# Kernel tuning notes

Hardware: AMD Instinct MI355X
Metric: run time of the kernel (lower is better)

The kernel has to match this reference:

```python
import jax, jax.numpy as jnp
import numpy as np

DIM, HEADS, DIM_HEAD = 256, 8, 32  # dim == heads * dim_head
EPS = 1e-5


def setup_inputs() -> dict:
    key = jax.random.key(0)
    ks = jax.random.split(key, 6)
    B, C, H, W = 16, DIM, 64, 64
    x = jax.random.normal(ks[0], (B, C, H, W), dtype=jnp.float32)
    # 1x1 conv weights stored as [out_ch, in_ch]
    w_qkv = jax.random.normal(ks[1], (3 * DIM, DIM), dtype=jnp.float32) * (1.0 / np.sqrt(DIM))
    w_out = jax.random.normal(ks[2], (DIM, DIM), dtype=jnp.float32) * (1.0 / np.sqrt(DIM))
    b_out = jax.random.normal(ks[3], (DIM,), dtype=jnp.float32) * 0.01
    ln_gamma = jnp.ones((DIM,), dtype=jnp.float32)
    ln_beta = jnp.zeros((DIM,), dtype=jnp.float32)
    return {"x": x, "w_qkv": w_qkv, "w_out": w_out, "b_out": b_out,
            "ln_gamma": ln_gamma, "ln_beta": ln_beta}


def _linear_attention(x, w_qkv, w_out, b_out, ln_gamma, ln_beta):
    B, C, H, W = x.shape
    d = C // HEADS
    # 1x1 conv == channel matmul
    qkv = jnp.einsum('bchw,oc->bohw', x, w_qkv)  # [B, 3C, H, W]
    q, k, v = jnp.split(qkv, 3, axis=1)
    # 'b (h d) x y -> b h x y d'
    def split_heads(t):
        t = t.reshape(B, HEADS, d, H, W)
        return t.transpose(0, 1, 3, 4, 2)  # b h x y d
    q, k, v = split_heads(q), split_heads(k), split_heads(v)
    q = jax.nn.softmax(q, axis=-1)   # over d (channel) dim
    k = jax.nn.softmax(k, axis=-2)   # over y spatial axis (faithful to torch dim=-2)
    context = jnp.einsum('bhxyd,bhxye->bhde', k, v)          # [B,H,d,d]
    out = jnp.einsum('bhde,bhxye->bhxyd', context, q)        # [B,H,X,Y,d]
    # 'b h x y d -> b (h d) x y'
    out = out.transpose(0, 1, 4, 2, 3).reshape(B, C, H, W)
    # output 1x1 conv + bias
    out = jnp.einsum('bchw,oc->bohw', out, w_out) + b_out[None, :, None, None]
    # LayerNorm over channel dim (permute to NHWC, norm last axis, permute back)
    y = out.transpose(0, 2, 3, 1)  # b h w c
    mu = jnp.mean(y, axis=-1, keepdims=True)
    var = jnp.var(y, axis=-1, keepdims=True)
    y = (y - mu) / jnp.sqrt(var + EPS) * ln_gamma + ln_beta
    return y.transpose(0, 3, 1, 2)


def reference(x, w_qkv, w_out, b_out, ln_gamma, ln_beta):
    return _linear_attention(x, w_qkv, w_out, b_out, ln_gamma, ln_beta)
```

## Files before the change

kernel.cpp:

```cpp
#include <hip/hip_runtime.h>
#include <hip/hip_bf16.h>

#define NB 16
#define CDIM 256
#define NHEADS 8
#define DH 32
#define NSP 4096
#define O3 768

typedef __bf16 bf16;
typedef bf16 bf16x4 __attribute__((ext_vector_type(4)));
typedef bf16 bf16x8 __attribute__((ext_vector_type(8)));
typedef float f32x4 __attribute__((ext_vector_type(4)));
typedef float f32x16 __attribute__((ext_vector_type(16)));

static __device__ __forceinline__ float bf2f(bf16 x){ return (float)x; }
static __device__ __forceinline__ bf16 f2bf(float x){ return (bf16)x; }

static __device__ __forceinline__ void gld16(const bf16* g, bf16* l){
    __builtin_amdgcn_global_load_lds((const __attribute__((address_space(1))) void*)g,
                                     (__attribute__((address_space(3))) void*)l, 16, 0, 0);
}

__global__ void k_transpose(const float* __restrict__ x, bf16* __restrict__ xT){
    __shared__ bf16 tile[64][72];
    int b = blockIdx.z;
    int c0 = blockIdx.y * 64;
    int n0 = blockIdx.x * 64;
    int t = threadIdx.x;
    const float* xb = x + (size_t)b * CDIM * NSP;
    #pragma unroll
    for (int i = 0; i < 4; ++i){
        int lin = i*256 + t;
        int c = lin >> 4;
        int n4 = (lin & 15) * 4;
        f32x4 f = *(const f32x4*)(xb + (size_t)(c0 + c)*NSP + n0 + n4);
        bf16x4 v4;
        #pragma unroll
        for (int j = 0; j < 4; ++j) v4[j] = f2bf(f[j]);
        *(bf16x4*)&tile[c][n4] = v4;
    }
    __syncthreads();
    bf16* xTb = xT + (size_t)b * NSP * CDIM;
    #pragma unroll
    for (int i = 0; i < 2; ++i){
        int lin = i*256 + t;
        int n = lin >> 3;
        int c8 = (lin & 7) * 8;
        bf16x8 v;
        #pragma unroll
        for (int j = 0; j < 8; ++j) v[j] = tile[c8+j][n];
        *(bf16x8*)(xTb + (size_t)(n0+n)*CDIM + c0 + c8) = v;
    }
}

__global__ void k_wcvt(const float* __restrict__ w, bf16* __restrict__ w2){
    int idx = (blockIdx.x*256 + threadIdx.x) * 4;
    f32x4 f = *(const f32x4*)(w + idx);
    bf16x4 v;
    #pragma unroll
    for (int j=0;j<4;j++) v[j] = f2bf(f[j]);
    *(bf16x4*)(w2 + idx) = v;
}

__global__ __launch_bounds__(1024,4) void k_kvctx(const bf16* __restrict__ w2,
                                                  const bf16* __restrict__ xT,
                                                  float* __restrict__ ctx_p){
    __shared__ union {
        bf16 Bs[32768];
        bf16 cb[32768];
    } sm;
    int bid = blockIdx.x;
    int xcd = bid & 7, slot = bid >> 3;
    int g = xcd*64 + slot;
    int b = g >> 5;
    int ntile = g & 31;
    int n0 = ntile * 128;
    int t = threadIdx.x;
    int wv = t >> 6, lane = t & 63;

    #pragma unroll
    for (int j=0;j<4;j++){
        int base_r = wv*8 + j*2;
        int r = base_r + (lane>>5);
        int c = (lane & 31) ^ (r & 7);
        gld16(xT + ((size_t)b*NSP + n0 + r)*CDIM + c*8, &sm.Bs[(size_t)base_r*256]);
    }
    __syncthreads();

    int brow[8], brx[8];
    #pragma unroll
    for (int ni=0;ni<8;ni++){
        int r = ni*16 + (lane&15);
        brow[ni] = r*32; brx[ni] = r & 7;
    }
    int arow = 256 + wv*32 + (lane&15);
    int acol = (lane>>4)*8;

    f32x4 acc[2][8];
    #pragma unroll
    for (int i=0;i<16;i++) ((f32x4*)acc)[i] = (f32x4){0.f,0.f,0.f,0.f};

    bf16x8 af0 = *(const bf16x8*)(w2 + (size_t)(arow     )*CDIM + acol);
    bf16x8 af1 = *(const bf16x8*)(w2 + (size_t)(arow + 16)*CDIM + acol);
    #pragma unroll
    for (int k0=0;k0<8;k0++){
        bf16x8 an0, an1;
        if (k0 < 7){
            an0 = *(const bf16x8*)(w2 + (size_t)(arow     )*CDIM + (k0+1)*32 + acol);
            an1 = *(const bf16x8*)(w2 + (size_t)(arow + 16)*CDIM + (k0+1)*32 + acol);
        }
        int cbase = (lane>>4) + k0*4;
        bf16x8 bfr[8];
        #pragma unroll
        for (int ni=0;ni<8;ni++)
            bfr[ni] = *(const bf16x8*)&sm.Bs[(size_t)(brow[ni] + (cbase ^ brx[ni]))*8];
        #pragma unroll
        for (int ni=0;ni<8;ni++)
            acc[0][ni] = __builtin_amdgcn_mfma_f32_16x16x32_bf16(af0, bfr[ni], acc[0][ni], 0, 0, 0);
        #pragma unroll
        for (int ni=0;ni<8;ni++)
            acc[1][ni] = __builtin_amdgcn_mfma_f32_16x16x32_bf16(af1, bfr[ni], acc[1][ni], 0, 0, 0);
        af0 = an0; af1 = an1;
    }

    if (wv < 8){
        #pragma unroll
        for (int mi=0;mi<2;mi++)
            #pragma unroll
            for (int r=0;r<4;r++)
                #pragma unroll
                for (int grp=0;grp<2;grp++){
                    float mx = -1e30f;
                    #pragma unroll
                    for (int q=0;q<4;q++) mx = fmaxf(mx, acc[mi][grp*4+q][r]);
                    #pragma unroll
                    for (int msk=1; msk<16; msk<<=1) mx = fmaxf(mx, __shfl_xor(mx, msk, 64));
                    float s = 0.f;
                    #pragma unroll
                    for (int q=0;q<4;q++){
                        float e = __expf(acc[mi][grp*4+q][r] - mx);
                        acc[mi][grp*4+q][r] = e; s += e;
                    }
                    #pragma unroll
                    for (int msk=1; msk<16; msk<<=1) s += __shfl_xor(s, msk, 64);
                    float inv = 1.f/s;
                    #pragma unroll
                    for (int q=0;q<4;q++) acc[mi][grp*4+q][r] *= inv;
                }
    }

    #pragma unroll
    for (int ph=0; ph<2; ++ph){
        __syncthreads();
        if (((wv>>2)&1) == ph){
            int isv  = wv >> 3;
            int w03  = wv & 3;
            int base = isv * 16384;
            #pragma unroll
            for (int mi=0;mi<2;mi++)
                #pragma unroll
                for (int ni=0;ni<8;ni++)
                    #pragma unroll
                    for (int r=0;r<4;r++){
                        int row = w03*32 + mi*16 + (lane>>4)*4 + r;
                        int n = ni*16 + (lane&15);
                        sm.cb[base + row*128 + (((n>>3) ^ (row&15))<<3) + (n&7)] = f2bf(acc[mi][ni][r]);
                    }
        }
        __syncthreads();
        if (wv < 4){
            f32x16 cacc;
            #pragma unroll
            for (int i=0;i<16;i++) cacc[i] = 0.f;
            int rr = wv*32 + (lane&31);
            #pragma unroll
            for (int s=0;s<8;s++){
                int nseg = s*2 + (lane>>5);
                int off = rr*128 + (((nseg ^ (rr&15))<<3));
                bf16x8 ka = *(const bf16x8*)&sm.cb[off];
                bf16x8 vb = *(const bf16x8*)&sm.cb[16384 + off];
                cacc = __builtin_amdgcn_mfma_f32_32x32x16_bf16(ka, vb, cacc, 0, 0, 0);
            }
            float* dst = ctx_p + ((size_t)(b*8 + ph*4 + wv)*32 + ntile)*1024;
            #pragma unroll
            for (int r=0;r<16;r++){
                int d = (r&3) + 8*(r>>2) + 4*(lane>>5);
                dst[d*32 + (lane&31)] = cacc[r];
            }
        }
    }
}

__global__ void k_merge(const float* __restrict__ w_out, const float* __restrict__ ctx_p,
                        bf16* __restrict__ W2){
    __shared__ float ctxs[32][32];
    int bh = blockIdx.x;
    int b = bh >> 3, h = bh & 7;
    int t = threadIdx.x;
    const float* base = ctx_p + (size_t)bh*32*1024;
    #pragma unroll
    for (int i=0;i<4;i++){
        int idx = i*256 + t;
        float s0 = 0.f, s1 = 0.f;
        #pragma unroll
        for (int p=0;p<16;p++){ s0 += base[(2*p)*1024 + idx]; s1 += base[(2*p+1)*1024 + idx]; }
        ((float*)ctxs)[idx] = s0 + s1;
    }
    __syncthreads();
    int o = t;
    const float* wrow = w_out + (size_t)o*CDIM + h*DH;
    float wv[32];
    #pragma unroll
    for (int d=0;d<32;d++) wv[d] = wrow[d];
    bf16* dst = W2 + ((size_t)b*CDIM + o)*CDIM + h*DH;
    #pragma unroll
    for (int g=0;g<4;g++){
        bf16x8 o8;
        #pragma unroll
        for (int jj=0;jj<8;jj++){
            int e = g*8 + jj;
            float s = 0.f;
            #pragma unroll
            for (int d=0;d<32;d++) s += wv[d]*ctxs[d][e];
            o8[jj] = f2bf(s);
        }
        *(bf16x8*)(dst + g*8) = o8;
    }
}

__global__ __launch_bounds__(256,4) void k_qout_ln(const bf16* __restrict__ w2,
                                                   const bf16* __restrict__ xT,
                                                   const bf16* __restrict__ W2,
                                                   const float* __restrict__ bout,
                                                   const float* __restrict__ gamma,
                                                   const float* __restrict__ beta,
                                                   float* __restrict__ out){
    __shared__ union {
        bf16 Bs[8192];
        float Yh[128*33];
    } sm;
    __shared__ float red[2][4][2][16];
    __shared__ float mu_s[32], rstd_s[32];
    int bid = blockIdx.x;
    int xcd = bid & 7, slot = bid >> 3;
    int b  = slot >> 4;
    int n0 = (xcd*16 + (slot & 15)) * 32;
    int t = threadIdx.x, wv = t>>6, lane = t&63;

    const bf16* xTb = xT + (size_t)b * NSP * CDIM;
    #pragma unroll
    for (int j=0;j<4;j++){
        int base_r = wv*8 + j*2;
        int r = base_r + (lane>>5);
        int c = (lane & 31) ^ (r & 7);
        gld16(xTb + (size_t)(n0 + r)*CDIM + c*8, &sm.Bs[(size_t)base_r*256]);
    }
    __syncthreads();

    int brow[2], brx[2];
    #pragma unroll
    for (int ni=0;ni<2;ni++){
        int r = ni*16 + (lane&15);
        brow[ni] = r*32; brx[ni] = r & 7;
    }
    int arow = wv*64 + (lane&15);
    int acol = (lane>>4)*8;

    f32x4 acc[4][2];
    #pragma unroll
    for (int i=0;i<8;i++) ((f32x4*)acc)[i] = (f32x4){0.f,0.f,0.f,0.f};
    {
        bf16x8 af[4], an[4];
        #pragma unroll
        for (int mi=0;mi<4;mi++)
            af[mi] = *(const bf16x8*)(w2 + (size_t)(arow + mi*16)*CDIM + acol);
        #pragma unroll
        for (int k0=0;k0<8;k0++){
            if (k0 < 7){
                #pragma unroll
                for (int mi=0;mi<4;mi++)
                    an[mi] = *(const bf16x8*)(w2 + (size_t)(arow + mi*16)*CDIM + (k0+1)*32 + acol);
            }
            int cbase = (lane>>4) + k0*4;
            bf16x8 bfr[2];
            #pragma unroll
            for (int ni=0;ni<2;ni++)
                bfr[ni] = *(const bf16x8*)&sm.Bs[(size_t)(brow[ni] + (cbase ^ brx[ni]))*8];
            #pragma unroll
            for (int mi=0;mi<4;mi++)
                #pragma unroll
                for (int ni=0;ni<2;ni++)
                    acc[mi][ni] = __builtin_amdgcn_mfma_f32_16x16x32_bf16(af[mi], bfr[ni], acc[mi][ni], 0, 0, 0);
            #pragma unroll
            for (int mi=0;mi<4;mi++) af[mi] = an[mi];
        }
    }

    #pragma unroll
    for (int ni=0;ni<2;ni++)
        #pragma unroll
        for (int hp=0;hp<2;hp++){
            float mx = -1e30f;
            #pragma unroll
            for (int mi=2*hp; mi<2*hp+2; mi++)
                #pragma unroll
                for (int r=0;r<4;r++) mx = fmaxf(mx, acc[mi][ni][r]);
            mx = fmaxf(mx, __shfl_xor(mx, 16, 64));
            mx = fmaxf(mx, __shfl_xor(mx, 32, 64));
            float s = 0.f;
            #pragma unroll
            for (int mi=2*hp; mi<2*hp+2; mi++)
                #pragma unroll
                for (int r=0;r<4;r++){
                    float e = __expf(acc[mi][ni][r] - mx);
                    acc[mi][ni][r] = e; s += e;
                }
            s += __shfl_xor(s, 16, 64);
            s += __shfl_xor(s, 32, 64);
            float inv = 1.f/s;
            #pragma unroll
            for (int mi=2*hp; mi<2*hp+2; mi++)
                #pragma unroll
                for (int r=0;r<4;r++) acc[mi][ni][r] *= inv;
        }

    __syncthreads();
    #pragma unroll
    for (int mi=0;mi<4;mi++)
        #pragma unroll
        for (int ni=0;ni<2;ni++){
            int n_loc = ni*16 + (lane&15);
            int cseg  = wv*8 + mi*2 + (lane>>5);
            bf16x4 v4;
            #pragma unroll
            for (int r=0;r<4;r++) v4[r] = f2bf(acc[mi][ni][r]);
            *(bf16x4*)&sm.Bs[(size_t)(n_loc*32 + (cseg ^ (n_loc&7)))*8 + ((lane>>4)&1)*4] = v4;
        }
    __syncthreads();

    const bf16* Ab = W2 + (size_t)b*CDIM*CDIM;
    f32x4 acc2[4][2];
    #pragma unroll
    for (int i=0;i<8;i++) ((f32x4*)acc2)[i] = (f32x4){0.f,0.f,0.f,0.f};
    {
        bf16x8 af[4], an[4];
        #pragma unroll
        for (int mi=0;mi<4;mi++)
            af[mi] = *(const bf16x8*)(Ab + (size_t)(arow + mi*16)*CDIM + acol);
        #pragma unroll
        for (int k0=0;k0<8;k0++){
            if (k0 < 7){
                #pragma unroll
                for (int mi=0;mi<4;mi++)
                    an[mi] = *(const bf16x8*)(Ab + (size_t)(arow + mi*16)*CDIM + (k0+1)*32 + acol);
            }
            int cbase = (lane>>4) + k0*4;
            bf16x8 bfr[2];
            #pragma unroll
            for (int ni=0;ni<2;ni++)
                bfr[ni] = *(const bf16x8*)&sm.Bs[(size_t)(brow[ni] + (cbase ^ brx[ni]))*8];
            #pragma unroll
            for (int mi=0;mi<4;mi++)
                #pragma unroll
                for (int ni=0;ni<2;ni++)
                    acc2[mi][ni] = __builtin_amdgcn_mfma_f32_16x16x32_bf16(af[mi], bfr[ni], acc2[mi][ni], 0, 0, 0);
            #pragma unroll
            for (int mi=0;mi<4;mi++) af[mi] = an[mi];
        }
    }

    float sA[2] = {0.f, 0.f}, sB[2] = {0.f, 0.f};
    #pragma unroll
    for (int mi=0;mi<4;mi++){
        f32x4 b4 = *(const f32x4*)&bout[wv*64 + mi*16 + (lane>>4)*4];
        #pragma unroll
        for (int ni=0;ni<2;ni++)
            #pragma unroll
            for (int r=0;r<4;r++){
                float y = acc2[mi][ni][r] + b4[r];
                acc2[mi][ni][r] = y;
                sA[ni] += y; sB[ni] += y*y;
            }
    }
    #pragma unroll
    for (int ni=0;ni<2;ni++){
        sA[ni] += __shfl_xor(sA[ni], 16, 64); sA[ni] += __shfl_xor(sA[ni], 32, 64);
        sB[ni] += __shfl_xor(sB[ni], 16, 64); sB[ni] += __shfl_xor(sB[ni], 32, 64);
    }
    if (lane < 16){
        #pragma unroll
        for (int ni=0;ni<2;ni++){
            red[0][wv][ni][lane] = sA[ni];
            red[1][wv][ni][lane] = sB[ni];
        }
    }
    __syncthreads();
    if (t < 32){
        float S = 0.f, S2 = 0.f;
        #pragma unroll
        for (int w=0;w<4;w++){ S += red[0][w][t>>4][t&15]; S2 += red[1][w][t>>4][t&15]; }
        float mu = S * (1.f/256.f);
        float var = S2*(1.f/256.f) - mu*mu;
        mu_s[t] = mu; rstd_s[t] = rsqrtf(var + 1e-5f);
    }
    __syncthreads();
    float mu[2], rs[2];
    #pragma unroll
    for (int ni=0;ni<2;ni++){
        mu[ni] = mu_s[ni*16 + (lane&15)];
        rs[ni] = rstd_s[ni*16 + (lane&15)];
    }
    #pragma unroll
    for (int mi=0;mi<4;mi++){
        int o0 = wv*64 + mi*16 + (lane>>4)*4;
        f32x4 g4  = *(const f32x4*)&gamma[o0];
        f32x4 be4 = *(const f32x4*)&beta[o0];
        #pragma unroll
        for (int ni=0;ni<2;ni++)
            #pragma unroll
            for (int r=0;r<4;r++)
                acc2[mi][ni][r] = (acc2[mi][ni][r] - mu[ni])*rs[ni]*g4[r] + be4[r];
    }

    size_t outb = (size_t)b*CDIM*NSP + n0;
    #pragma unroll
    for (int p=0; p<2; ++p){
        __syncthreads();
        #pragma unroll
        for (int mi=2*p; mi<2*p+2; mi++)
            #pragma unroll
            for (int ni=0;ni<2;ni++){
                int row = wv*32 + (mi&1)*16 + (lane>>4)*4;
                int n = ni*16 + (lane&15);
                #pragma unroll
                for (int r=0;r<4;r++) sm.Yh[(row+r)*33 + n] = acc2[mi][ni][r];
            }
        __syncthreads();
        int n = t & 31, q = t >> 5;
        #pragma unroll
        for (int i=0;i<16;i++){
            int row = q*16 + i;
            int o_act = (row>>5)*64 + p*32 + (row&31);
            out[outb + (size_t)o_act*NSP + n] = sm.Yh[row*33 + n];
        }
    }
}

extern "C" void kernel_launch(void* const* d_in, const int* in_sizes, int n_in,
                              void* d_out, int out_size, void* d_ws, size_t ws_size,
                              hipStream_t stream){
    const float* x     = (const float*)d_in[0];
    const float* w_qkv = (const float*)d_in[1];
    const float* w_out = (const float*)d_in[2];
    const float* b_out = (const float*)d_in[3];
    const float* gamma = (const float*)d_in[4];
    const float* beta  = (const float*)d_in[5];
    float* out = (float*)d_out;
    char* ws = (char*)d_ws;
    bf16*  xT    = (bf16*) ws;
    float* ctx_p = (float*)(ws + 67108864ull);
    bf16*  W2    = (bf16*)(ws + 134742016ull);
    bf16*  w2    = (bf16*)(ws + 136839168ull);

    k_wcvt     <<<dim3(192),       256,  0, stream>>>(w_qkv, w2);
    k_transpose<<<dim3(64, 4, NB), 256,  0, stream>>>(x, xT);
    k_kvctx    <<<dim3(512),       1024, 0, stream>>>(w2, xT, ctx_p);
    k_merge    <<<dim3(128),       256,  0, stream>>>(w_out, ctx_p, W2);
    k_qout_ln  <<<dim3(2048),      256,  0, stream>>>(w2, xT, W2, b_out, gamma, beta, out);
}
```

Measured before the change: 234.4 us.

## Widen qout_ln tiles to 64 spatial columns with 512-thread blocks

The fused q-projection/softmax/output/LayerNorm kernel now handles 64 spatial positions per block with 8 waves, each owning 32 output channels (one head) instead of 64. Each A-fragment load of w2 and W2 from global memory now feeds twice as many MFMAs, and the grid is halved. The merge kernel also goes to 512 threads, splitting each output row's columns across two halves. The cost is more LDS per block (the Bs and Yh buffers double), lower occupancy bounds, and a two-phase output store in which only half the waves write on each pass.

Result: faster. 210.0 us (-10.4%).

```diff
diff --git a/kernel.cpp b/kernel.cpp
--- a/kernel.cpp
+++ b/kernel.cpp
@@ -200,26 +200,26 @@
     int t = threadIdx.x;
     const float* base = ctx_p + (size_t)bh*32*1024;
     #pragma unroll
-    for (int i=0;i<4;i++){
-        int idx = i*256 + t;
+    for (int i=0;i<2;i++){
+        int idx = i*512 + t;
         float s0 = 0.f, s1 = 0.f;
         #pragma unroll
         for (int p=0;p<16;p++){ s0 += base[(2*p)*1024 + idx]; s1 += base[(2*p+1)*1024 + idx]; }
         ((float*)ctxs)[idx] = s0 + s1;
     }
     __syncthreads();
-    int o = t;
+    int o = t & 255, half = t >> 8;
     const float* wrow = w_out + (size_t)o*CDIM + h*DH;
     float wv[32];
     #pragma unroll
     for (int d=0;d<32;d++) wv[d] = wrow[d];
-    bf16* dst = W2 + ((size_t)b*CDIM + o)*CDIM + h*DH;
-    #pragma unroll
-    for (int g=0;g<4;g++){
+    bf16* dst = W2 + ((size_t)b*CDIM + o)*CDIM + h*DH + half*16;
+    #pragma unroll
+    for (int g=0;g<2;g++){
         bf16x8 o8;
         #pragma unroll
         for (int jj=0;jj<8;jj++){
-            int e = g*8 + jj;
+            int e = half*16 + g*8 + jj;
             float s = 0.f;
             #pragma unroll
             for (int d=0;d<32;d++) s += wv[d]*ctxs[d][e];
@@ -229,7 +229,7 @@
     }
 }
 
-__global__ __launch_bounds__(256,4) void k_qout_ln(const bf16* __restrict__ w2,
+__global__ __launch_bounds__(512,2) void k_qout_ln(const bf16* __restrict__ w2,
                                                    const bf16* __restrict__ xT,
                                                    const bf16* __restrict__ W2,
                                                    const float* __restrict__ bout,
@@ -237,15 +237,16 @@
                                                    const float* __restrict__ beta,
                                                    float* __restrict__ out){
     __shared__ union {
-        bf16 Bs[8192];
-        float Yh[128*33];
+        bf16 Bs[16384];
+        float Yh[128*65];
     } sm;
-    __shared__ float red[2][4][2][16];
-    __shared__ float mu_s[32], rstd_s[32];
+    __shared__ float red[2][8][4][16];
+    __shared__ float mu_s[64], rstd_s[64];
     int bid = blockIdx.x;
     int xcd = bid & 7, slot = bid >> 3;
-    int b  = slot >> 4;
-    int n0 = (xcd*16 + (slot & 15)) * 32;
+    int g = xcd*128 + slot;
+    int b  = g >> 6;
+    int n0 = (g & 63) * 64;
     int t = threadIdx.x, wv = t>>6, lane = t&63;
 
     const bf16* xTb = xT + (size_t)b * NSP * CDIM;
@@ -258,80 +259,78 @@
     }
     __syncthreads();
 
-    int brow[2], brx[2];
-    #pragma unroll
-    for (int ni=0;ni<2;ni++){
+    int brow[4], brx[4];
+    #pragma unroll
+    for (int ni=0;ni<4;ni++){
         int r = ni*16 + (lane&15);
         brow[ni] = r*32; brx[ni] = r & 7;
     }
-    int arow = wv*64 + (lane&15);
+    int arow = wv*32 + (lane&15);
     int acol = (lane>>4)*8;
 
-    f32x4 acc[4][2];
+    f32x4 acc[2][4];
     #pragma unroll
     for (int i=0;i<8;i++) ((f32x4*)acc)[i] = (f32x4){0.f,0.f,0.f,0.f};
     {
-        bf16x8 af[4], an[4];
-        #pragma unroll
-        for (int mi=0;mi<4;mi++)
+        bf16x8 af[2], an[2];
+        #pragma unroll
+        for (int mi=0;mi<2;mi++)
             af[mi] = *(const bf16x8*)(w2 + (size_t)(arow + mi*16)*CDIM + acol);
         #pragma unroll
         for (int k0=0;k0<8;k0++){
             if (k0 < 7){
                 #pragma unroll
-                for (int mi=0;mi<4;mi++)
+                for (int mi=0;mi<2;mi++)
                     an[mi] = *(const bf16x8*)(w2 + (size_t)(arow + mi*16)*CDIM + (k0+1)*32 + acol);
             }
             int cbase = (lane>>4) + k0*4;
-            bf16x8 bfr[2];
-            #pragma unroll
-            for (int ni=0;ni<2;ni++)
+            bf16x8 bfr[4];
+            #pragma unroll
+            for (int ni=0;ni<4;ni++)
                 bfr[ni] = *(const bf16x8*)&sm.Bs[(size_t)(brow[ni] + (cbase ^ brx[ni]))*8];
             #pragma unroll
-            for (int mi=0;mi<4;mi++)
-                #pragma unroll
-                for (int ni=0;ni<2;ni++)
+            for (int mi=0;mi<2;mi++)
+                #pragma unroll
+                for (int ni=0;ni<4;ni++)
                     acc[mi][ni] = __builtin_amdgcn_mfma_f32_16x16x32_bf16(af[mi], bfr[ni], acc[mi][ni], 0, 0, 0);
             #pragma unroll
-            for (int mi=0;mi<4;mi++) af[mi] = an[mi];
-        }
-    }
-
-    #pragma unroll
-    for (int ni=0;ni<2;ni++)
-        #pragma unroll
-        for (int hp=0;hp<2;hp++){
-            float mx = -1e30f;
-            #pragma unroll
-            for (int mi=2*hp; mi<2*hp+2; mi++)
-                #pragma unroll
-                for (int r=0;r<4;r++) mx = fmaxf(mx, acc[mi][ni][r]);
-            mx = fmaxf(mx, __shfl_xor(mx, 16, 64));
-            mx = fmaxf(mx, __shfl_xor(mx, 32, 64));
-            float s = 0.f;
-            #pragma unroll
-            for (int mi=2*hp; mi<2*hp+2; mi++)
-                #pragma unroll
-                for (int r=0;r<4;r++){
-                    float e = __expf(acc[mi][ni][r] - mx);
-                    acc[mi][ni][r] = e; s += e;
-                }
-            s += __shfl_xor(s, 16, 64);
-            s += __shfl_xor(s, 32, 64);
-            float inv = 1.f/s;
-            #pragma unroll
-            for (int mi=2*hp; mi<2*hp+2; mi++)
-                #pragma unroll
-                for (int r=0;r<4;r++) acc[mi][ni][r] *= inv;
-        }
-
-    __syncthreads();
-    #pragma unroll
-    for (int mi=0;mi<4;mi++)
-        #pragma unroll
-        for (int ni=0;ni<2;ni++){
+            for (int mi=0;mi<2;mi++) af[mi] = an[mi];
+        }
+    }
+
+    #pragma unroll
+    for (int ni=0;ni<4;ni++){
+        float mx = -1e30f;
+        #pragma unroll
+        for (int mi=0;mi<2;mi++)
+            #pragma unroll
+            for (int r=0;r<4;r++) mx = fmaxf(mx, acc[mi][ni][r]);
+        mx = fmaxf(mx, __shfl_xor(mx, 16, 64));
+        mx = fmaxf(mx, __shfl_xor(mx, 32, 64));
+        float s = 0.f;
+        #pragma unroll
+        for (int mi=0;mi<2;mi++)
+            #pragma unroll
+            for (int r=0;r<4;r++){
+                float e = __expf(acc[mi][ni][r] - mx);
+                acc[mi][ni][r] = e; s += e;
+            }
+        s += __shfl_xor(s, 16, 64);
+        s += __shfl_xor(s, 32, 64);
+        float inv = 1.f/s;
+        #pragma unroll
+        for (int mi=0;mi<2;mi++)
+            #pragma unroll
+            for (int r=0;r<4;r++) acc[mi][ni][r] *= inv;
+    }
+
+    __syncthreads();
+    #pragma unroll
+    for (int mi=0;mi<2;mi++)
+        #pragma unroll
+        for (int ni=0;ni<4;ni++){
             int n_loc = ni*16 + (lane&15);
-            int cseg  = wv*8 + mi*2 + (lane>>5);
+            int cseg  = wv*4 + mi*2 + ((lane>>4)>>1);
             bf16x4 v4;
             #pragma unroll
             for (int r=0;r<4;r++) v4[r] = f2bf(acc[mi][ni][r]);
@@ -340,42 +339,42 @@
     __syncthreads();
 
     const bf16* Ab = W2 + (size_t)b*CDIM*CDIM;
-    f32x4 acc2[4][2];
+    f32x4 acc2[2][4];
     #pragma unroll
     for (int i=0;i<8;i++) ((f32x4*)acc2)[i] = (f32x4){0.f,0.f,0.f,0.f};
     {
-        bf16x8 af[4], an[4];
-        #pragma unroll
-        for (int mi=0;mi<4;mi++)
+        bf16x8 af[2], an[2];
+        #pragma unroll
+        for (int mi=0;mi<2;mi++)
             af[mi] = *(const bf16x8*)(Ab + (size_t)(arow + mi*16)*CDIM + acol);
         #pragma unroll
         for (int k0=0;k0<8;k0++){
             if (k0 < 7){
                 #pragma unroll
-                for (int mi=0;mi<4;mi++)
+                for (int mi=0;mi<2;mi++)
                     an[mi] = *(const bf16x8*)(Ab + (size_t)(arow + mi*16)*CDIM + (k0+1)*32 + acol);
             }
             int cbase = (lane>>4) + k0*4;
-            bf16x8 bfr[2];
-            #pragma unroll
-            for (int ni=0;ni<2;ni++)
+            bf16x8 bfr[4];
+            #pragma unroll
+            for (int ni=0;ni<4;ni++)
                 bfr[ni] = *(const bf16x8*)&sm.Bs[(size_t)(brow[ni] + (cbase ^ brx[ni]))*8];
             #pragma unroll
-            for (int mi=0;mi<4;mi++)
-                #pragma unroll
-                for (int ni=0;ni<2;ni++)
+            for (int mi=0;mi<2;mi++)
+                #pragma unroll
+                for (int ni=0;ni<4;ni++)
                     acc2[mi][ni] = __builtin_amdgcn_mfma_f32_16x16x32_bf16(af[mi], bfr[ni], acc2[mi][ni], 0, 0, 0);
             #pragma unroll
-            for (int mi=0;mi<4;mi++) af[mi] = an[mi];
-        }
-    }
-
-    float sA[2] = {0.f, 0.f}, sB[2] = {0.f, 0.f};
-    #pragma unroll
-    for (int mi=0;mi<4;mi++){
-        f32x4 b4 = *(const f32x4*)&bout[wv*64 + mi*16 + (lane>>4)*4];
-        #pragma unroll
-        for (int ni=0;ni<2;ni++)
+            for (int mi=0;mi<2;mi++) af[mi] = an[mi];
+        }
+    }
+
+    float sA[4] = {0.f,0.f,0.f,0.f}, sB[4] = {0.f,0.f,0.f,0.f};
+    #pragma unroll
+    for (int mi=0;mi<2;mi++){
+        f32x4 b4 = *(const f32x4*)&bout[wv*32 + mi*16 + (lane>>4)*4];
+        #pragma unroll
+        for (int ni=0;ni<4;ni++)
             #pragma unroll
             for (int r=0;r<4;r++){
                 float y = acc2[mi][ni][r] + b4[r];
@@ -384,40 +383,40 @@
             }
     }
     #pragma unroll
-    for (int ni=0;ni<2;ni++){
+    for (int ni=0;ni<4;ni++){
         sA[ni] += __shfl_xor(sA[ni], 16, 64); sA[ni] += __shfl_xor(sA[ni], 32, 64);
         sB[ni] += __shfl_xor(sB[ni], 16, 64); sB[ni] += __shfl_xor(sB[ni], 32, 64);
     }
     if (lane < 16){
         #pragma unroll
-        for (int ni=0;ni<2;ni++){
+        for (int ni=0;ni<4;ni++){
             red[0][wv][ni][lane] = sA[ni];
             red[1][wv][ni][lane] = sB[ni];
         }
     }
     __syncthreads();
-    if (t < 32){
+    if (t < 64){
         float S = 0.f, S2 = 0.f;
         #pragma unroll
-        for (int w=0;w<4;w++){ S += red[0][w][t>>4][t&15]; S2 += red[1][w][t>>4][t&15]; }
+        for (int w=0;w<8;w++){ S += red[0][w][t>>4][t&15]; S2 += red[1][w][t>>4][t&15]; }
         float mu = S * (1.f/256.f);
         float var = S2*(1.f/256.f) - mu*mu;
         mu_s[t] = mu; rstd_s[t] = rsqrtf(var + 1e-5f);
     }
     __syncthreads();
-    float mu[2], rs[2];
-    #pragma unroll
-    for (int ni=0;ni<2;ni++){
+    float mu[4], rs[4];
+    #pragma unroll
+    for (int ni=0;ni<4;ni++){
         mu[ni] = mu_s[ni*16 + (lane&15)];
         rs[ni] = rstd_s[ni*16 + (lane&15)];
     }
     #pragma unroll
-    for (int mi=0;mi<4;mi++){
-        int o0 = wv*64 + mi*16 + (lane>>4)*4;
+    for (int mi=0;mi<2;mi++){
+        int o0 = wv*32 + mi*16 + (lane>>4)*4;
         f32x4 g4  = *(const f32x4*)&gamma[o0];
         f32x4 be4 = *(const f32x4*)&beta[o0];
         #pragma unroll
-        for (int ni=0;ni<2;ni++)
+        for (int ni=0;ni<4;ni++)
             #pragma unroll
             for (int r=0;r<4;r++)
                 acc2[mi][ni][r] = (acc2[mi][ni][r] - mu[ni])*rs[ni]*g4[r] + be4[r];
@@ -427,22 +426,23 @@
     #pragma unroll
     for (int p=0; p<2; ++p){
         __syncthreads();
-        #pragma unroll
-        for (int mi=2*p; mi<2*p+2; mi++)
-            #pragma unroll
-            for (int ni=0;ni<2;ni++){
-                int row = wv*32 + (mi&1)*16 + (lane>>4)*4;
-                int n = ni*16 + (lane&15);
-                #pragma unroll
-                for (int r=0;r<4;r++) sm.Yh[(row+r)*33 + n] = acc2[mi][ni][r];
-            }
+        if ((wv>>2) == p){
+            #pragma unroll
+            for (int mi=0;mi<2;mi++)
+                #pragma unroll
+                for (int ni=0;ni<4;ni++){
+                    int row = (wv&3)*32 + mi*16 + (lane>>4)*4;
+                    int n = ni*16 + (lane&15);
+                    #pragma unroll
+                    for (int r=0;r<4;r++) sm.Yh[(row+r)*65 + n] = acc2[mi][ni][r];
+                }
+        }
         __syncthreads();
-        int n = t & 31, q = t >> 5;
+        int n = t & 63, q = t >> 6;
         #pragma unroll
         for (int i=0;i<16;i++){
             int row = q*16 + i;
-            int o_act = (row>>5)*64 + p*32 + (row&31);
-            out[outb + (size_t)o_act*NSP + n] = sm.Yh[row*33 + n];
+            out[outb + (size_t)(p*128 + row)*NSP + n] = sm.Yh[row*65 + n];
         }
     }
 }
@@ -466,6 +466,6 @@
     k_wcvt     <<<dim3(192),       256,  0, stream>>>(w_qkv, w2);
     k_transpose<<<dim3(64, 4, NB), 256,  0, stream>>>(x, xT);
     k_kvctx    <<<dim3(512),       1024, 0, stream>>>(w2, xT, ctx_p);
-    k_merge    <<<dim3(128),       256,  0, stream>>>(w_out, ctx_p, W2);
-    k_qout_ln  <<<dim3(2048),      256,  0, stream>>>(w2, xT, W2, b_out, gamma, beta, out);
-}
+    k_merge    <<<dim3(128),       512,  0, stream>>>(w_out, ctx_p, W2);
+    k_qout_ln  <<<dim3(1024),      512,  0, stream>>>(w2, xT, W2, b_out, gamma, beta, out);
+}
```
